# Kernel tuning notes

Measured on AMD Instinct MI355X. Metric: run time of the kernel, lower is better.

Reference implementation:

```python
import jax, jax.numpy as jnp
import numpy as np

THRESHOLD = 0.02  # matches init threshold
N_POINTS = 4_000_000
N_PLANES = 64


def setup_inputs() -> dict:
    key = jax.random.key(0)
    k1, k2, k3 = jax.random.split(key, 3)
    points = jax.random.uniform(k1, (N_POINTS, 3), dtype=jnp.float32)
    normals = jax.random.normal(k2, (N_PLANES, 3), dtype=jnp.float32)
    normals = normals / jnp.linalg.norm(normals, axis=1, keepdims=True)
    # anchor each plane at a random point inside the cube so it intersects the cloud
    anchors = jax.random.uniform(k3, (N_PLANES, 3), dtype=jnp.float32)
    distances = jnp.sum(normals * anchors, axis=1)
    return {"points": points, "normals": normals, "distances": distances}


def reference(points, normals, distances):
    """Sequential per-plane SVD refinement + masked projection (faithful to torch loop).

    Plane fits (mask, centroid, covariance) use the ORIGINAL points, as in the
    source; only the projection is applied cumulatively to the running state.
    """
    dtype = points.dtype
    jitter = jnp.diag(jnp.asarray([1.0, 2.0, 3.0], dtype))  # keeps eigh well-posed for invalid planes

    def step(proj, plane):
        n, d = plane
        # inlier mask on original points (data-dependent in torch; here a weight vector)
        m = (jnp.abs(points @ n - d) < THRESHOLD).astype(dtype)  # (N,)
        cnt = jnp.sum(m)
        validf = (cnt >= 3.0).astype(dtype)
        centroid = jnp.sum(m[:, None] * points, axis=0) / jnp.maximum(cnt, 1.0)  # (3,)
        xc = (points - centroid) * m[:, None]  # masked centered points (N,3)
        cov = xc.T @ xc  # (3,3), m is 0/1 so single weighting == mask-select
        cov = cov + (1.0 - validf) * jitter
        # smallest-eigenvalue eigenvector of symmetric cov == torch V[:, 2] (up to sign)
        _, V = jnp.linalg.eigh(cov)
        rn = V[:, 0]
        rn = jnp.where(jnp.dot(rn, n) < 0.0, -rn, rn)  # align with coarse normal
        rd = jnp.dot(centroid, rn)
        # project only masked points of the running state onto refined plane
        delta = (proj @ rn - rd)[:, None] * rn[None, :]  # (N,3)
        proj = proj - (validf * m)[:, None] * delta
        return proj, None

    proj, _ = jax.lax.scan(step, points, (normals, distances))
    return proj
```

## Files before the change

kernel.cpp:

```cpp
#include <hip/hip_runtime.h>
#include <math.h>

#define N_POINTS 4000000
#define N_PLANES 64
#define THRESH   0.02f
#define NVALS    (N_PLANES*10)
#define RBLOCKS  1024
#define RTHREADS 512
#define UB       16

__global__ __launch_bounds__(RTHREADS)
void reduce_kernel(const float* __restrict__ pts,
                   const float* __restrict__ nrm,
                   const float* __restrict__ dst,
                   float* __restrict__ partials, int ppw)
{
    const int lane = threadIdx.x & 63;
    const int wid  = __builtin_amdgcn_readfirstlane((int)(threadIdx.x >> 6));
    const int gwave = blockIdx.x * (RTHREADS / 64) + wid;

    const float nx = nrm[lane*3+0];
    const float ny = nrm[lane*3+1];
    const float nz = nrm[lane*3+2];
    const float nd = -dst[lane];

    float cnt=0.f, sx=0.f, sy=0.f, sz=0.f;
    float xx=0.f, xy=0.f, xz=0.f, yy=0.f, yz=0.f, zz=0.f;

    long long beg = (long long)gwave * ppw;
    long long end = beg + ppw;
    if (beg > N_POINTS) beg = N_POINTS;
    if (end > N_POINTS) end = N_POINTS;

    long long j = beg;
    for (; j + UB <= end; j += UB) {
        float X[UB], Y[UB], Z[UB];
#pragma unroll
        for (int u = 0; u < UB; ++u) {
            X[u] = pts[(j+u)*3+0];
            Y[u] = pts[(j+u)*3+1];
            Z[u] = pts[(j+u)*3+2];
        }
#pragma unroll
        for (int u = 0; u < UB; ++u) {
            const float t  = fmaf(X[u], nx, fmaf(Y[u], ny, fmaf(Z[u], nz, nd)));
            const float fm = (fabsf(t) < THRESH) ? 1.0f : 0.0f;
            const float tx = fm * X[u], ty = fm * Y[u], tz = fm * Z[u];
            cnt += fm;
            sx += tx; sy += ty; sz += tz;
            xx = fmaf(tx, X[u], xx); xy = fmaf(tx, Y[u], xy); xz = fmaf(tx, Z[u], xz);
            yy = fmaf(ty, Y[u], yy); yz = fmaf(ty, Z[u], yz); zz = fmaf(tz, Z[u], zz);
        }
    }
    for (; j < end; ++j) {
        const float x = pts[j*3+0];
        const float y = pts[j*3+1];
        const float z = pts[j*3+2];
        const float t  = fmaf(x, nx, fmaf(y, ny, fmaf(z, nz, nd)));
        const float fm = (fabsf(t) < THRESH) ? 1.0f : 0.0f;
        const float tx = fm * x, ty = fm * y, tz = fm * z;
        cnt += fm;
        sx += tx; sy += ty; sz += tz;
        xx = fmaf(tx, x, xx); xy = fmaf(tx, y, xy); xz = fmaf(tx, z, xz);
        yy = fmaf(ty, y, yy); yz = fmaf(ty, z, yz); zz = fmaf(tz, z, zz);
    }

    __shared__ float part[RTHREADS/64][NVALS];
    {
        float* r = &part[threadIdx.x >> 6][lane * 10];
        r[0]=cnt; r[1]=sx; r[2]=sy; r[3]=sz;
        r[4]=xx; r[5]=xy; r[6]=xz; r[7]=yy; r[8]=yz; r[9]=zz;
    }
    __syncthreads();
    for (int v = threadIdx.x; v < NVALS; v += RTHREADS) {
        float s = 0.f;
#pragma unroll
        for (int w = 0; w < RTHREADS/64; ++w) s += part[w][v];
        partials[(long long)blockIdx.x * NVALS + v] = s;
    }
}

__global__ __launch_bounds__(256)
void finalize_kernel(const float* __restrict__ partials, int nb,
                     const float* __restrict__ nrm,
                     const float* __restrict__ dst,
                     float* __restrict__ params)
{
    const int p    = blockIdx.x;
    const int lane = threadIdx.x & 63;
    const int wid  = threadIdx.x >> 6;

    double s[10];
#pragma unroll
    for (int q = 0; q < 10; ++q) s[q] = 0.0;

    for (int b = threadIdx.x; b < nb; b += 256) {
        const float* row = partials + (long long)b * NVALS + p * 10;
#pragma unroll
        for (int q = 0; q < 10; ++q) s[q] += (double)row[q];
    }

#pragma unroll
    for (int off = 32; off; off >>= 1)
#pragma unroll
        for (int q = 0; q < 10; ++q) s[q] += __shfl_xor(s[q], off);

    __shared__ double wsum[4][10];
    if (lane == 0) {
#pragma unroll
        for (int q = 0; q < 10; ++q) wsum[wid][q] = s[q];
    }
    __syncthreads();
    if (threadIdx.x != 0) return;

    double a[10];
#pragma unroll
    for (int q = 0; q < 10; ++q)
        a[q] = wsum[0][q] + wsum[1][q] + wsum[2][q] + wsum[3][q];

    const double cnt = a[0];
    const double sx = a[1], sy = a[2], sz = a[3];
    const double den = fmax(cnt, 1.0);
    const double cx = sx / den, cy = sy / den, cz = sz / den;

    double C[3][3];
    C[0][0] = a[4] - 2.0*cx*sx + cnt*cx*cx;
    C[0][1] = a[5] - cx*sy - cy*sx + cnt*cx*cy;
    C[0][2] = a[6] - cx*sz - cz*sx + cnt*cx*cz;
    C[1][1] = a[7] - 2.0*cy*sy + cnt*cy*cy;
    C[1][2] = a[8] - cy*sz - cz*sy + cnt*cy*cz;
    C[2][2] = a[9] - 2.0*cz*sz + cnt*cz*cz;
    C[1][0] = C[0][1]; C[2][0] = C[0][2]; C[2][1] = C[1][2];

    const double valid = (cnt >= 3.0) ? 1.0 : 0.0;
    C[0][0] += (1.0 - valid) * 1.0;
    C[1][1] += (1.0 - valid) * 2.0;
    C[2][2] += (1.0 - valid) * 3.0;

    double V[3][3] = {{1,0,0},{0,1,0},{0,0,1}};
    for (int sweep = 0; sweep < 15; ++sweep) {
#pragma unroll
        for (int k = 0; k < 3; ++k) {
            const int pp = (k == 2) ? 1 : 0;
            const int qq = (k == 0) ? 1 : 2;
            const int rr = 3 - pp - qq;
            const double apq = C[pp][qq];
            if (fabs(apq) < 1e-300) continue;
            const double theta = (C[qq][qq] - C[pp][pp]) / (2.0 * apq);
            const double t = copysign(1.0, theta) / (fabs(theta) + sqrt(theta*theta + 1.0));
            const double c = 1.0 / sqrt(t*t + 1.0);
            const double ss = t * c;
            const double app = C[pp][pp], aqq = C[qq][qq];
            const double arp = C[rr][pp], arq = C[rr][qq];
            C[pp][pp] = app - t * apq;
            C[qq][qq] = aqq + t * apq;
            C[pp][qq] = 0.0; C[qq][pp] = 0.0;
            const double nrp = c*arp - ss*arq;
            const double nrq = ss*arp + c*arq;
            C[rr][pp] = nrp; C[pp][rr] = nrp;
            C[rr][qq] = nrq; C[qq][rr] = nrq;
#pragma unroll
            for (int i = 0; i < 3; ++i) {
                const double vip = V[i][pp], viq = V[i][qq];
                V[i][pp] = c*vip - ss*viq;
                V[i][qq] = ss*vip + c*viq;
            }
        }
    }

    int idx = 0;
    if (C[1][1] < C[idx][idx]) idx = 1;
    if (C[2][2] < C[idx][idx]) idx = 2;
    double rx = V[0][idx], ry = V[1][idx], rz = V[2][idx];
    const double inv = 1.0 / sqrt(rx*rx + ry*ry + rz*rz);
    rx *= inv; ry *= inv; rz *= inv;

    const double nxd = (double)nrm[p*3+0];
    const double nyd = (double)nrm[p*3+1];
    const double nzd = (double)nrm[p*3+2];
    if (rx*nxd + ry*nyd + rz*nzd < 0.0) { rx = -rx; ry = -ry; rz = -rz; }
    const double rd = cx*rx + cy*ry + cz*rz;

    const float vldf = (float)valid;
    params[p*8+0] = nrm[p*3+0];
    params[p*8+1] = nrm[p*3+1];
    params[p*8+2] = nrm[p*3+2];
    params[p*8+3] = -dst[p];
    params[p*8+4] = vldf * (float)rx;
    params[p*8+5] = vldf * (float)ry;
    params[p*8+6] = vldf * (float)rz;
    params[p*8+7] = -(vldf * (float)rd);
}

#define PPTH 4
#define PQ   (N_POINTS / PPTH)

__global__ __launch_bounds__(256)
void project_kernel(const float* __restrict__ pts,
                    const float* __restrict__ params,
                    float* __restrict__ out)
{
    const int tid = blockIdx.x * 256 + threadIdx.x;
    if (tid >= PQ) return;

    float ox[PPTH], oy[PPTH], oz[PPTH];
    float qx[PPTH], qy[PPTH], qz[PPTH];
#pragma unroll
    for (int k = 0; k < PPTH; ++k) {
        const long long i = (long long)tid + (long long)k * PQ;
        ox[k] = pts[i*3+0]; oy[k] = pts[i*3+1]; oz[k] = pts[i*3+2];
        qx[k] = ox[k]; qy[k] = oy[k]; qz[k] = oz[k];
    }

#pragma unroll 2
    for (int p = 0; p < N_PLANES; ++p) {
        const float nx  = params[p*8+0];
        const float ny  = params[p*8+1];
        const float nz  = params[p*8+2];
        const float md  = params[p*8+3];
        const float rvx = params[p*8+4];
        const float rvy = params[p*8+5];
        const float rvz = params[p*8+6];
        const float mrd = params[p*8+7];

#pragma unroll
        for (int k = 0; k < PPTH; ++k) {
            const float t0 = fmaf(ox[k], nx, fmaf(oy[k], ny, fmaf(oz[k], nz, md)));
            const float t  = fmaf(qx[k], rvx, fmaf(qy[k], rvy, fmaf(qz[k], rvz, mrd)));
            const float tm = (fabsf(t0) < THRESH) ? t : 0.0f;
            qx[k] = fmaf(-tm, rvx, qx[k]);
            qy[k] = fmaf(-tm, rvy, qy[k]);
            qz[k] = fmaf(-tm, rvz, qz[k]);
        }
    }

#pragma unroll
    for (int k = 0; k < PPTH; ++k) {
        const long long i = (long long)tid + (long long)k * PQ;
        out[i*3+0] = qx[k];
        out[i*3+1] = qy[k];
        out[i*3+2] = qz[k];
    }
}

extern "C" void kernel_launch(void* const* d_in, const int* in_sizes, int n_in,
                              void* d_out, int out_size, void* d_ws, size_t ws_size,
                              hipStream_t stream)
{
    const float* pts = (const float*)d_in[0];
    const float* nrm = (const float*)d_in[1];
    const float* dst = (const float*)d_in[2];
    float* out = (float*)d_out;

    size_t avail = (ws_size > 8192) ? (ws_size - 8192) : 0;
    int nb = (int)(avail / (NVALS * sizeof(float)));
    if (nb < 1) nb = 1;
    if (nb > RBLOCKS) nb = RBLOCKS;

    float* partials = (float*)d_ws;
    size_t poff = ((size_t)nb * NVALS * sizeof(float) + 255) & ~(size_t)255;
    float* params = (float*)((char*)d_ws + poff);

    const int nwaves = nb * (RTHREADS / 64);
    const int ppw = (int)((N_POINTS + nwaves - 1) / nwaves);

    hipLaunchKernelGGL(reduce_kernel, dim3(nb), dim3(RTHREADS), 0, stream,
                       pts, nrm, dst, partials, ppw);
    hipLaunchKernelGGL(finalize_kernel, dim3(N_PLANES), dim3(256), 0, stream,
                       partials, nb, nrm, dst, params);
    hipLaunchKernelGGL(project_kernel, dim3((PQ + 255) / 256), dim3(256), 0, stream,
                       pts, params, out);
}
```

Before: 201.4 us.

## Double-buffer point loads in reduce kernel and retune block shape

```diff
diff --git a/kernel.cpp b/kernel.cpp
--- a/kernel.cpp
+++ b/kernel.cpp
@@ -5,9 +5,42 @@
 #define N_PLANES 64
 #define THRESH   0.02f
 #define NVALS    (N_PLANES*10)
-#define RBLOCKS  1024
-#define RTHREADS 512
-#define UB       16
+#define RBLOCKS  2048
+#define RTHREADS 256
+#define UB       8
+
+__device__ __forceinline__
+void load_batch(const float* __restrict__ pts, int b,
+                float (&X)[UB], float (&Y)[UB], float (&Z)[UB])
+{
+#pragma unroll
+    for (int u = 0; u < UB; ++u) {
+        int ix = b + u;
+        ix = (ix < N_POINTS) ? ix : (N_POINTS - 1);
+        X[u] = pts[ix*3+0];
+        Y[u] = pts[ix*3+1];
+        Z[u] = pts[ix*3+2];
+    }
+}
+
+__device__ __forceinline__
+void comp_batch(const float (&X)[UB], const float (&Y)[UB], const float (&Z)[UB],
+                float nx, float ny, float nz, float nd,
+                float& cnt, float& sx, float& sy, float& sz,
+                float& xx, float& xy, float& xz,
+                float& yy, float& yz, float& zz)
+{
+#pragma unroll
+    for (int u = 0; u < UB; ++u) {
+        const float t  = fmaf(X[u], nx, fmaf(Y[u], ny, fmaf(Z[u], nz, nd)));
+        const float fm = (fabsf(t) < THRESH) ? 1.0f : 0.0f;
+        const float tx = fm * X[u], ty = fm * Y[u], tz = fm * Z[u];
+        cnt += fm;
+        sx += tx; sy += ty; sz += tz;
+        xx = fmaf(tx, X[u], xx); xy = fmaf(tx, Y[u], xy); xz = fmaf(tx, Z[u], xz);
+        yy = fmaf(ty, Y[u], yy); yz = fmaf(ty, Z[u], yz); zz = fmaf(tz, Z[u], zz);
+    }
+}
 
 __global__ __launch_bounds__(RTHREADS)
 void reduce_kernel(const float* __restrict__ pts,
@@ -17,7 +50,7 @@
 {
     const int lane = threadIdx.x & 63;
     const int wid  = __builtin_amdgcn_readfirstlane((int)(threadIdx.x >> 6));
-    const int gwave = blockIdx.x * (RTHREADS / 64) + wid;
+    const int gwave = blockIdx.x * (RTHREADS/64) + wid;
 
     const float nx = nrm[lane*3+0];
     const float ny = nrm[lane*3+1];
@@ -27,30 +60,24 @@
     float cnt=0.f, sx=0.f, sy=0.f, sz=0.f;
     float xx=0.f, xy=0.f, xz=0.f, yy=0.f, yz=0.f, zz=0.f;
 
-    long long beg = (long long)gwave * ppw;
-    long long end = beg + ppw;
-    if (beg > N_POINTS) beg = N_POINTS;
-    if (end > N_POINTS) end = N_POINTS;
-
-    long long j = beg;
-    for (; j + UB <= end; j += UB) {
-        float X[UB], Y[UB], Z[UB];
-#pragma unroll
-        for (int u = 0; u < UB; ++u) {
-            X[u] = pts[(j+u)*3+0];
-            Y[u] = pts[(j+u)*3+1];
-            Z[u] = pts[(j+u)*3+2];
-        }
-#pragma unroll
-        for (int u = 0; u < UB; ++u) {
-            const float t  = fmaf(X[u], nx, fmaf(Y[u], ny, fmaf(Z[u], nz, nd)));
-            const float fm = (fabsf(t) < THRESH) ? 1.0f : 0.0f;
-            const float tx = fm * X[u], ty = fm * Y[u], tz = fm * Z[u];
-            cnt += fm;
-            sx += tx; sy += ty; sz += tz;
-            xx = fmaf(tx, X[u], xx); xy = fmaf(tx, Y[u], xy); xz = fmaf(tx, Z[u], xz);
-            yy = fmaf(ty, Y[u], yy); yz = fmaf(ty, Z[u], yz); zz = fmaf(tz, Z[u], zz);
-        }
+    int beg = gwave * ppw; if (beg > N_POINTS) beg = N_POINTS;
+    int end = beg + ppw;   if (end > N_POINTS) end = N_POINTS;
+
+    float XA[UB], YA[UB], ZA[UB], XB[UB], YB[UB], ZB[UB];
+
+    int j = beg;
+    if (j + UB <= end)
+        load_batch(pts, j, XA, YA, ZA);
+
+    for (; j + 2*UB <= end; j += 2*UB) {
+        load_batch(pts, j + UB, XB, YB, ZB);
+        comp_batch(XA, YA, ZA, nx, ny, nz, nd, cnt, sx, sy, sz, xx, xy, xz, yy, yz, zz);
+        load_batch(pts, j + 2*UB, XA, YA, ZA);
+        comp_batch(XB, YB, ZB, nx, ny, nz, nd, cnt, sx, sy, sz, xx, xy, xz, yy, yz, zz);
+    }
+    if (j + UB <= end) {
+        comp_batch(XA, YA, ZA, nx, ny, nz, nd, cnt, sx, sy, sz, xx, xy, xz, yy, yz, zz);
+        j += UB;
     }
     for (; j < end; ++j) {
         const float x = pts[j*3+0];
```

Result: slower. 210.4 us (+4.5%).

## Load point chunks coalesced per wave and broadcast via readlane in reduction

Applied to the files above, without the earlier changes.

```diff
diff --git a/kernel.cpp b/kernel.cpp
--- a/kernel.cpp
+++ b/kernel.cpp
@@ -5,77 +5,104 @@
 #define N_PLANES 64
 #define THRESH   0.02f
 #define NVALS    (N_PLANES*10)
-#define RBLOCKS  1024
-#define RTHREADS 512
-#define UB       16
+#define RBLOCKS  2048
+#define RTHREADS 256
+#define NCHUNK   (N_POINTS/64)
+
+__device__ __forceinline__ float rlane(float v, int i) {
+    return __uint_as_float(__builtin_amdgcn_readlane(__float_as_uint(v), i));
+}
+__device__ __forceinline__ unsigned uminu(unsigned a, unsigned b) {
+    return a < b ? a : b;
+}
+
+struct Acc {
+    float cnt, sx, sy, sz, xx, xy, xz, yy, yz, zz;
+};
+
+__device__ __forceinline__
+void compute_chunk(float vx, float vy, float vz,
+                   float nx, float ny, float nz, float nd, Acc& a)
+{
+#pragma unroll 1
+    for (int g = 0; g < 64; g += 16) {
+#pragma unroll
+        for (int k = 0; k < 16; ++k) {
+            const float x = rlane(vx, g + k);
+            const float y = rlane(vy, g + k);
+            const float z = rlane(vz, g + k);
+            const float t  = fmaf(x, nx, fmaf(y, ny, fmaf(z, nz, nd)));
+            const float fm = (fabsf(t) < THRESH) ? 1.0f : 0.0f;
+            const float tx = fm * x, ty = fm * y, tz = fm * z;
+            a.cnt += fm;
+            a.sx += tx; a.sy += ty; a.sz += tz;
+            a.xx = fmaf(tx, x, a.xx); a.xy = fmaf(tx, y, a.xy); a.xz = fmaf(tx, z, a.xz);
+            a.yy = fmaf(ty, y, a.yy); a.yz = fmaf(ty, z, a.yz); a.zz = fmaf(tz, z, a.zz);
+        }
+    }
+}
 
 __global__ __launch_bounds__(RTHREADS)
 void reduce_kernel(const float* __restrict__ pts,
                    const float* __restrict__ nrm,
                    const float* __restrict__ dst,
-                   float* __restrict__ partials, int ppw)
+                   float* __restrict__ partials, int nwaves)
 {
     const int lane = threadIdx.x & 63;
-    const int wid  = __builtin_amdgcn_readfirstlane((int)(threadIdx.x >> 6));
-    const int gwave = blockIdx.x * (RTHREADS / 64) + wid;
+    const int wid  = threadIdx.x >> 6;
+    const int w    = blockIdx.x * (RTHREADS/64) + wid;
 
     const float nx = nrm[lane*3+0];
     const float ny = nrm[lane*3+1];
     const float nz = nrm[lane*3+2];
     const float nd = -dst[lane];
 
-    float cnt=0.f, sx=0.f, sy=0.f, sz=0.f;
-    float xx=0.f, xy=0.f, xz=0.f, yy=0.f, yz=0.f, zz=0.f;
-
-    long long beg = (long long)gwave * ppw;
-    long long end = beg + ppw;
-    if (beg > N_POINTS) beg = N_POINTS;
-    if (end > N_POINTS) end = N_POINTS;
-
-    long long j = beg;
-    for (; j + UB <= end; j += UB) {
-        float X[UB], Y[UB], Z[UB];
-#pragma unroll
-        for (int u = 0; u < UB; ++u) {
-            X[u] = pts[(j+u)*3+0];
-            Y[u] = pts[(j+u)*3+1];
-            Z[u] = pts[(j+u)*3+2];
-        }
-#pragma unroll
-        for (int u = 0; u < UB; ++u) {
-            const float t  = fmaf(X[u], nx, fmaf(Y[u], ny, fmaf(Z[u], nz, nd)));
-            const float fm = (fabsf(t) < THRESH) ? 1.0f : 0.0f;
-            const float tx = fm * X[u], ty = fm * Y[u], tz = fm * Z[u];
-            cnt += fm;
-            sx += tx; sy += ty; sz += tz;
-            xx = fmaf(tx, X[u], xx); xy = fmaf(tx, Y[u], xy); xz = fmaf(tx, Z[u], xz);
-            yy = fmaf(ty, Y[u], yy); yz = fmaf(ty, Z[u], yz); zz = fmaf(tz, Z[u], zz);
-        }
-    }
-    for (; j < end; ++j) {
-        const float x = pts[j*3+0];
-        const float y = pts[j*3+1];
-        const float z = pts[j*3+2];
-        const float t  = fmaf(x, nx, fmaf(y, ny, fmaf(z, nz, nd)));
-        const float fm = (fabsf(t) < THRESH) ? 1.0f : 0.0f;
-        const float tx = fm * x, ty = fm * y, tz = fm * z;
-        cnt += fm;
-        sx += tx; sy += ty; sz += tz;
-        xx = fmaf(tx, x, xx); xy = fmaf(tx, y, xy); xz = fmaf(tx, z, xz);
-        yy = fmaf(ty, y, yy); yz = fmaf(ty, z, yz); zz = fmaf(tz, z, zz);
-    }
+    const int cpw  = NCHUNK / nwaves;
+    const int rem  = NCHUNK % nwaves;
+    const int cbeg = w * cpw + (w < rem ? w : rem);
+    const int cc   = cpw + (w < rem ? 1 : 0);
+
+    Acc a = {0.f,0.f,0.f,0.f,0.f,0.f,0.f,0.f,0.f,0.f};
+
+    const char* base = (const char*)pts;
+    const unsigned offmax = (unsigned)(NCHUNK-1) * 768u + (unsigned)lane * 12u;
+    unsigned offA = uminu((unsigned)cbeg * 768u + (unsigned)lane * 12u, offmax);
+
+    float ax, ay, az, bx, by, bz;
+    ax = *(const float*)(base + offA + 0);
+    ay = *(const float*)(base + offA + 4);
+    az = *(const float*)(base + offA + 8);
+    unsigned offB = uminu(offA + 768u, offmax);
+
+    int c = 0;
+    while (c + 2 <= cc) {
+        bx = *(const float*)(base + offB + 0);
+        by = *(const float*)(base + offB + 4);
+        bz = *(const float*)(base + offB + 8);
+        compute_chunk(ax, ay, az, nx, ny, nz, nd, a);
+        const unsigned offA2 = uminu(offB + 768u, offmax);
+        ax = *(const float*)(base + offA2 + 0);
+        ay = *(const float*)(base + offA2 + 4);
+        az = *(const float*)(base + offA2 + 8);
+        compute_chunk(bx, by, bz, nx, ny, nz, nd, a);
+        offA = offA2;
+        offB = uminu(offA2 + 768u, offmax);
+        c += 2;
+    }
+    if (c < cc)
+        compute_chunk(ax, ay, az, nx, ny, nz, nd, a);
 
     __shared__ float part[RTHREADS/64][NVALS];
     {
-        float* r = &part[threadIdx.x >> 6][lane * 10];
-        r[0]=cnt; r[1]=sx; r[2]=sy; r[3]=sz;
-        r[4]=xx; r[5]=xy; r[6]=xz; r[7]=yy; r[8]=yz; r[9]=zz;
+        float* r = &part[wid][lane * 10];
+        r[0]=a.cnt; r[1]=a.sx; r[2]=a.sy; r[3]=a.sz;
+        r[4]=a.xx;  r[5]=a.xy; r[6]=a.xz; r[7]=a.yy; r[8]=a.yz; r[9]=a.zz;
     }
     __syncthreads();
     for (int v = threadIdx.x; v < NVALS; v += RTHREADS) {
         float s = 0.f;
 #pragma unroll
-        for (int w = 0; w < RTHREADS/64; ++w) s += part[w][v];
+        for (int ww = 0; ww < RTHREADS/64; ++ww) s += part[ww][v];
         partials[(long long)blockIdx.x * NVALS + v] = s;
     }
 }
@@ -113,23 +140,23 @@
     __syncthreads();
     if (threadIdx.x != 0) return;
 
-    double a[10];
+    double acc[10];
 #pragma unroll
     for (int q = 0; q < 10; ++q)
-        a[q] = wsum[0][q] + wsum[1][q] + wsum[2][q] + wsum[3][q];
-
-    const double cnt = a[0];
-    const double sx = a[1], sy = a[2], sz = a[3];
+        acc[q] = wsum[0][q] + wsum[1][q] + wsum[2][q] + wsum[3][q];
+
+    const double cnt = acc[0];
+    const double sx = acc[1], sy = acc[2], sz = acc[3];
     const double den = fmax(cnt, 1.0);
     const double cx = sx / den, cy = sy / den, cz = sz / den;
 
     double C[3][3];
-    C[0][0] = a[4] - 2.0*cx*sx + cnt*cx*cx;
-    C[0][1] = a[5] - cx*sy - cy*sx + cnt*cx*cy;
-    C[0][2] = a[6] - cx*sz - cz*sx + cnt*cx*cz;
-    C[1][1] = a[7] - 2.0*cy*sy + cnt*cy*cy;
-    C[1][2] = a[8] - cy*sz - cz*sy + cnt*cy*cz;
-    C[2][2] = a[9] - 2.0*cz*sz + cnt*cz*cz;
+    C[0][0] = acc[4] - 2.0*cx*sx + cnt*cx*cx;
+    C[0][1] = acc[5] - cx*sy - cy*sx + cnt*cx*cy;
+    C[0][2] = acc[6] - cx*sz - cz*sx + cnt*cx*cz;
+    C[1][1] = acc[7] - 2.0*cy*sy + cnt*cy*cy;
+    C[1][2] = acc[8] - cy*sz - cz*sy + cnt*cy*cz;
+    C[2][2] = acc[9] - 2.0*cz*sz + cnt*cz*cz;
     C[1][0] = C[0][1]; C[2][0] = C[0][2]; C[2][1] = C[1][2];
 
     const double valid = (cnt >= 3.0) ? 1.0 : 0.0;
@@ -212,7 +239,7 @@
         qx[k] = ox[k]; qy[k] = oy[k]; qz[k] = oz[k];
     }
 
-#pragma unroll 2
+#pragma unroll 4
     for (int p = 0; p < N_PLANES; ++p) {
         const float nx  = params[p*8+0];
         const float ny  = params[p*8+1];
@@ -262,10 +289,9 @@
     float* params = (float*)((char*)d_ws + poff);
 
     const int nwaves = nb * (RTHREADS / 64);
-    const int ppw = (int)((N_POINTS + nwaves - 1) / nwaves);
 
     hipLaunchKernelGGL(reduce_kernel, dim3(nb), dim3(RTHREADS), 0, stream,
-                       pts, nrm, dst, partials, ppw);
+                       pts, nrm, dst, partials, nwaves);
     hipLaunchKernelGGL(finalize_kernel, dim3(N_PLANES), dim3(256), 0, stream,
                        partials, nb, nrm, dst, params);
     hipLaunchKernelGGL(project_kernel, dim3((PQ + 255) / 256), dim3(256), 0, stream,
```

After: 235.8 us. 17.1% more time.
